# Performance work log

Hardware: AMD Instinct MI355X
Metric: run time of the kernel (lower is better)

## Reference

```python
import jax, jax.numpy as jnp
import numpy as np

B, L, E, H, DK, DV = 4, 2048, 512, 8, 64, 64
NEG = -1e9
LN_EPS = 1e-5


def setup_inputs() -> dict:
    key = jax.random.key(0)
    ks = jax.random.split(key, 16)
    q = jax.random.normal(ks[0], (B, L, E), jnp.float32)
    k = jax.random.normal(ks[1], (B, L, E), jnp.float32)
    v = jax.random.normal(ks[2], (B, L, E), jnp.float32)
    mask = jax.random.randint(ks[3], (B, L, L), 0, 2) > 0  # True = masked position
    def lin(kk, fan_in, dout, din):
        W = jax.random.normal(kk, (dout, din), jnp.float32) * (1.0 / np.sqrt(din))
        b = jnp.zeros((dout,), jnp.float32)
        return W, b
    Wq, bq = lin(ks[4], E, H * DK, E)
    Wk, bk = lin(ks[5], E, H * DK, E)
    Wv, bv = lin(ks[6], E, H * DV, E)
    Wfc, bfc = lin(ks[7], H * DV, E, H * DV)
    gamma = jnp.ones((E,), jnp.float32)
    beta = jnp.zeros((E,), jnp.float32)
    return dict(q=q, k=k, v=v, mask=mask, Wq=Wq, bq=bq, Wk=Wk, bk=bk,
                Wv=Wv, bv=bv, Wfc=Wfc, bfc=bfc, gamma=gamma, beta=beta)


def reference(q, k, v, mask, Wq, bq, Wk, bk, Wv, bv, Wfc, bfc, gamma, beta):
    residual = q
    Bq, Lq, _ = q.shape
    Lk = k.shape[1]
    # QKV projections, split heads: [B, L, H, D]
    qh = (q @ Wq.T + bq).reshape(Bq, Lq, H, DK)
    kh = (k @ Wk.T + bk).reshape(Bq, Lk, H, DK)
    vh = (v @ Wv.T + bv).reshape(Bq, Lk, H, DV)
    temp = jnp.asarray(np.sqrt(DK), qh.dtype)
    # scores in torch layout [H, B, Lq, Lk] (heads fastest-varying in H*B flatten)
    scores = jnp.einsum('bqhd,bkhd->hbqk', qh, kh) / temp
    scores = jnp.where(mask[None, :, :, :], NEG, scores)  # mask repeated over heads
    attn = jax.nn.softmax(scores, axis=-1)
    out = jnp.einsum('hbqk,bkhd->bqhd', attn, vh).reshape(Bq, Lq, H * DV)
    out = out @ Wfc.T + bfc
    # dropout p=0 -> identity
    x = out + residual
    mu = jnp.mean(x, axis=-1, keepdims=True)
    var = jnp.var(x, axis=-1, keepdims=True)
    outputs = (x - mu) / jnp.sqrt(var + LN_EPS) * gamma + beta
    attns = attn.reshape(H * Bq, Lq, Lk)
    return outputs, attns
```

## Files before the change

### kernel.cpp

```cpp
#include <hip/hip_runtime.h>

#define B_ 4
#define L_ 2048
#define E_ 512
#define H_ 8
#define D_ 64
#define NEGV (-1e9f)

typedef short s8v __attribute__((ext_vector_type(8)));
typedef float f4v __attribute__((ext_vector_type(4)));

static __device__ __forceinline__ unsigned short f2bf(float f) {
    union { float f; unsigned u; } v; v.f = f;
    unsigned r = v.u + 0x7FFFu + ((v.u >> 16) & 1u);
    return (unsigned short)(r >> 16);
}

template<int MODE, bool ABF16>
__global__ __launch_bounds__(256)
void gemm_bt(const void* __restrict__ Aptr, int lda,
             const float* __restrict__ Bm, int ldb,
             const float* __restrict__ bias,
             const float* __restrict__ resid,
             void* __restrict__ Cout, int ldc)
{
    constexpr int LS = 40;
    __shared__ unsigned short As[128 * LS];
    __shared__ unsigned short Bs[128 * LS];
    const int t = threadIdx.x;
    const int lane = t & 63, w = t >> 6;
    const int wm = (w >> 1) * 64, wn = (w & 1) * 64;
    const int bm0 = blockIdx.x * 128, bn0 = blockIdx.y * 128;
    const int ar = t >> 1, ak = (t & 1) * 16;
    const int fr = lane & 15, fq = lane >> 4, fk = fq * 8;

    f4v zero = {0.f, 0.f, 0.f, 0.f};
    f4v acc[4][4];
#pragma unroll
    for (int i = 0; i < 4; i++)
#pragma unroll
        for (int j = 0; j < 4; j++) acc[i][j] = zero;

    for (int k0 = 0; k0 < E_; k0 += 32) {
        unsigned short ta[16], tb[16];
        if (ABF16) {
            const unsigned short* ag = (const unsigned short*)Aptr + (size_t)(bm0 + ar) * lda + k0 + ak;
            *(int4*)&ta[0] = *(const int4*)ag;
            *(int4*)&ta[8] = *(const int4*)(ag + 8);
        } else {
            const float* ag = (const float*)Aptr + (size_t)(bm0 + ar) * lda + k0 + ak;
#pragma unroll
            for (int u = 0; u < 16; u += 4) {
                float4 va = *(const float4*)(ag + u);
                ta[u] = f2bf(va.x); ta[u+1] = f2bf(va.y);
                ta[u+2] = f2bf(va.z); ta[u+3] = f2bf(va.w);
            }
        }
        {
            const float* bg = Bm + (size_t)(bn0 + ar) * ldb + k0 + ak;
#pragma unroll
            for (int u = 0; u < 16; u += 4) {
                float4 vb = *(const float4*)(bg + u);
                tb[u] = f2bf(vb.x); tb[u+1] = f2bf(vb.y);
                tb[u+2] = f2bf(vb.z); tb[u+3] = f2bf(vb.w);
            }
        }
        __syncthreads();
        *(int4*)&As[ar * LS + ak]     = *(int4*)&ta[0];
        *(int4*)&As[ar * LS + ak + 8] = *(int4*)&ta[8];
        *(int4*)&Bs[ar * LS + ak]     = *(int4*)&tb[0];
        *(int4*)&Bs[ar * LS + ak + 8] = *(int4*)&tb[8];
        __syncthreads();

        s8v af[4], bf[4];
#pragma unroll
        for (int i = 0; i < 4; i++) af[i] = *(const s8v*)&As[(wm + 16*i + fr) * LS + fk];
#pragma unroll
        for (int j = 0; j < 4; j++) bf[j] = *(const s8v*)&Bs[(wn + 16*j + fr) * LS + fk];
#pragma unroll
        for (int i = 0; i < 4; i++)
#pragma unroll
            for (int j = 0; j < 4; j++)
                acc[i][j] = __builtin_amdgcn_mfma_f32_16x16x32_bf16(af[i], bf[j], acc[i][j], 0, 0, 0);
    }

#pragma unroll
    for (int i = 0; i < 4; i++) {
#pragma unroll
        for (int j = 0; j < 4; j++) {
            const int col = bn0 + wn + 16*j + fr;
            const float bv = bias ? bias[col] : 0.f;
#pragma unroll
            for (int reg = 0; reg < 4; reg++) {
                const int row = bm0 + wm + 16*i + fq*4 + reg;
                float val = acc[i][j][reg] + bv;
                if (MODE == 0) {
                    ((unsigned short*)Cout)[(size_t)row * ldc + col] = f2bf(val);
                } else if (MODE == 1) {
                    const int b = row >> 11, lk = row & 2047;
                    const int h = col >> 6,  dv = col & 63;
                    ((unsigned short*)Cout)[(((size_t)(b * H_ + h) * 64 + dv) << 11) + lk] = f2bf(val);
                } else {
                    float o = val + resid[(size_t)row * ldc + col];
                    ((float*)Cout)[(size_t)row * ldc + col] = o;
                }
            }
        }
    }
}

__global__ __launch_bounds__(256)
void attn_p1(const unsigned short* __restrict__ qh,
             const unsigned short* __restrict__ kh,
             const int* __restrict__ mask,
             float* __restrict__ stat_m, float* __restrict__ stat_l)
{
    __shared__ unsigned short Qs[64 * 72];
    __shared__ unsigned short Ks[128 * 72];
    const int t = threadIdx.x, lane = t & 63, w = t >> 6;
    const int q0 = blockIdx.x * 64;
    const int bh = blockIdx.y, b = bh >> 3, h = bh & 7;
    const int fr = lane & 15, fq = lane >> 4, fk = fq * 8;
    f4v zero = {0.f, 0.f, 0.f, 0.f};

    {
        const int row = t >> 2, kofs = (t & 3) * 16;
        const unsigned short* g = qh + ((size_t)(b * L_ + q0 + row) * E_ + h * 64 + kofs);
        *(int4*)&Qs[row * 72 + kofs]     = *(const int4*)g;
        *(int4*)&Qs[row * 72 + kofs + 8] = *(const int4*)(g + 8);
    }

    float m_r[4], l_r[4];
#pragma unroll
    for (int r = 0; r < 4; r++) { m_r[r] = -3e38f; l_r[r] = 0.f; }

    const size_t mbase = (size_t)b * ((size_t)L_ * L_);

    for (int kb = 0; kb < L_; kb += 128) {
        __syncthreads();
        {
            const int row = t >> 1, kofs = (t & 1) * 32;
            const unsigned short* g = kh + ((size_t)(b * L_ + kb + row) * E_ + h * 64 + kofs);
#pragma unroll
            for (int u = 0; u < 4; u++)
                *(int4*)&Ks[row * 72 + kofs + u * 8] = *(const int4*)(g + u * 8);
        }
        __syncthreads();

        s8v aq0 = *(const s8v*)&Qs[(w * 16 + fr) * 72 + fk];
        s8v aq1 = *(const s8v*)&Qs[(w * 16 + fr) * 72 + 32 + fk];
        f4v sv[8];
#pragma unroll
        for (int nt = 0; nt < 8; nt++) {
            s8v b0 = *(const s8v*)&Ks[(nt * 16 + fr) * 72 + fk];
            s8v b1 = *(const s8v*)&Ks[(nt * 16 + fr) * 72 + 32 + fk];
            f4v sc = zero;
            sc = __builtin_amdgcn_mfma_f32_16x16x32_bf16(aq0, b0, sc, 0, 0, 0);
            sc = __builtin_amdgcn_mfma_f32_16x16x32_bf16(aq1, b1, sc, 0, 0, 0);
            sv[nt] = sc;
        }

        float tm[4] = {-3e38f, -3e38f, -3e38f, -3e38f};
#pragma unroll
        for (int nt = 0; nt < 8; nt++)
#pragma unroll
            for (int reg = 0; reg < 4; reg++) {
                const int row = q0 + w * 16 + fq * 4 + reg;
                const int col = kb + nt * 16 + fr;
                const int mk = mask[mbase + (size_t)row * L_ + col];
                float s = mk ? NEGV : sv[nt][reg] * 0.125f;
                sv[nt][reg] = s;
                tm[reg] = fmaxf(tm[reg], s);
            }
#pragma unroll
        for (int d = 1; d < 16; d <<= 1)
#pragma unroll
            for (int reg = 0; reg < 4; reg++)
                tm[reg] = fmaxf(tm[reg], __shfl_xor(tm[reg], d));
#pragma unroll
        for (int reg = 0; reg < 4; reg++) {
            const float mn = fmaxf(m_r[reg], tm[reg]);
            const float corr = __expf(m_r[reg] - mn);
            float ps = 0.f;
#pragma unroll
            for (int nt = 0; nt < 8; nt++) ps += __expf(sv[nt][reg] - mn);
#pragma unroll
            for (int d = 1; d < 16; d <<= 1) ps += __shfl_xor(ps, d);
            l_r[reg] = l_r[reg] * corr + ps;
            m_r[reg] = mn;
        }
    }

    if (fr == 0) {
#pragma unroll
        for (int reg = 0; reg < 4; reg++) {
            const int row = q0 + w * 16 + fq * 4 + reg;
            stat_m[(size_t)bh * L_ + row] = m_r[reg];
            stat_l[(size_t)bh * L_ + row] = l_r[reg];
        }
    }
}

__global__ __launch_bounds__(256)
void attn_p2(const unsigned short* __restrict__ qh,
             const unsigned short* __restrict__ kh,
             const unsigned short* __restrict__ vt,
             const int* __restrict__ mask,
             const float* __restrict__ stat_m, const float* __restrict__ stat_l,
             float* __restrict__ attns, unsigned short* __restrict__ oh)
{
    __shared__ unsigned short Qs[64 * 72];
    __shared__ unsigned short Ks[128 * 72];
    __shared__ unsigned short Vs[64 * 136];
    __shared__ unsigned short Ps[64 * 136];
    const int t = threadIdx.x, lane = t & 63, w = t >> 6;
    const int q0 = blockIdx.x * 64;
    const int bh = blockIdx.y, b = bh >> 3, h = bh & 7;
    const int fr = lane & 15, fq = lane >> 4, fk = fq * 8;
    f4v zero = {0.f, 0.f, 0.f, 0.f};

    {
        const int row = t >> 2, kofs = (t & 3) * 16;
        const unsigned short* g = qh + ((size_t)(b * L_ + q0 + row) * E_ + h * 64 + kofs);
        *(int4*)&Qs[row * 72 + kofs]     = *(const int4*)g;
        *(int4*)&Qs[row * 72 + kofs + 8] = *(const int4*)(g + 8);
    }

    float m_r[4], rl[4];
#pragma unroll
    for (int reg = 0; reg < 4; reg++) {
        const int row = q0 + w * 16 + fq * 4 + reg;
        m_r[reg] = stat_m[(size_t)bh * L_ + row];
        rl[reg]  = 1.f / stat_l[(size_t)bh * L_ + row];
    }

    f4v o[4];
#pragma unroll
    for (int j = 0; j < 4; j++) o[j] = zero;

    const size_t mbase = (size_t)b * ((size_t)L_ * L_);
    const size_t abase = (size_t)(h * B_ + b) * ((size_t)L_ * L_);
    const int prow = w * 16 + fq * 4;

    for (int kb = 0; kb < L_; kb += 128) {
        __syncthreads();
        {
            const int row = t >> 1, kofs = (t & 1) * 32;
            const unsigned short* g = kh + ((size_t)(b * L_ + kb + row) * E_ + h * 64 + kofs);
#pragma unroll
            for (int u = 0; u < 4; u++)
                *(int4*)&Ks[row * 72 + kofs + u * 8] = *(const int4*)(g + u * 8);
        }
        {
            const int row = t >> 2, kofs = (t & 3) * 32;
            const unsigned short* g = vt + ((size_t)(b * H_ + h) * 64 + row) * L_ + kb + kofs;
#pragma unroll
            for (int u = 0; u < 4; u++)
                *(int4*)&Vs[row * 136 + kofs + u * 8] = *(const int4*)(g + u * 8);
        }
        __syncthreads();

        s8v aq0 = *(const s8v*)&Qs[(w * 16 + fr) * 72 + fk];
        s8v aq1 = *(const s8v*)&Qs[(w * 16 + fr) * 72 + 32 + fk];
#pragma unroll
        for (int nt = 0; nt < 8; nt++) {
            s8v b0 = *(const s8v*)&Ks[(nt * 16 + fr) * 72 + fk];
            s8v b1 = *(const s8v*)&Ks[(nt * 16 + fr) * 72 + 32 + fk];
            f4v sc = zero;
            sc = __builtin_amdgcn_mfma_f32_16x16x32_bf16(aq0, b0, sc, 0, 0, 0);
            sc = __builtin_amdgcn_mfma_f32_16x16x32_bf16(aq1, b1, sc, 0, 0, 0);
#pragma unroll
            for (int reg = 0; reg < 4; reg++) {
                const int row = q0 + prow + reg;
                const int col = kb + nt * 16 + fr;
                const int mk = mask[mbase + (size_t)row * L_ + col];
                float s = mk ? NEGV : sc[reg] * 0.125f;
                float p = __expf(s - m_r[reg]) * rl[reg];
                __builtin_nontemporal_store(p, &attns[abase + (size_t)row * L_ + col]);
                Ps[(prow + reg) * 136 + nt * 16 + fr] = f2bf(p);
            }
        }
        __syncthreads();

#pragma unroll
        for (int ks = 0; ks < 4; ks++) {
            s8v pa = *(const s8v*)&Ps[(w * 16 + fr) * 136 + ks * 32 + fk];
#pragma unroll
            for (int j = 0; j < 4; j++) {
                s8v vb = *(const s8v*)&Vs[(j * 16 + fr) * 136 + ks * 32 + fk];
                o[j] = __builtin_amdgcn_mfma_f32_16x16x32_bf16(pa, vb, o[j], 0, 0, 0);
            }
        }
    }

#pragma unroll
    for (int j = 0; j < 4; j++)
#pragma unroll
        for (int reg = 0; reg < 4; reg++) {
            const int row = q0 + prow + reg;
            const int col = h * 64 + j * 16 + fr;
            oh[(size_t)(b * L_ + row) * (H_ * D_) + col] = f2bf(o[j][reg]);
        }
}

__global__ __launch_bounds__(256)
void ln_k(const float* __restrict__ x, const float* __restrict__ gamma,
          const float* __restrict__ beta, float* __restrict__ out)
{
    const int t = threadIdx.x, lane = t & 63, w = t >> 6;
    const int row = blockIdx.x * 4 + w;
    const float* xr = x + (size_t)row * E_;
    const int cb = lane * 8;
    float4 a = *(const float4*)(xr + cb);
    float4 c = *(const float4*)(xr + cb + 4);
    float s  = a.x + a.y + a.z + a.w + c.x + c.y + c.z + c.w;
    float s2 = a.x*a.x + a.y*a.y + a.z*a.z + a.w*a.w
             + c.x*c.x + c.y*c.y + c.z*c.z + c.w*c.w;
#pragma unroll
    for (int d = 1; d < 64; d <<= 1) { s += __shfl_xor(s, d); s2 += __shfl_xor(s2, d); }
    const float mu  = s * (1.f / E_);
    const float var = s2 * (1.f / E_) - mu * mu;
    const float rs  = rsqrtf(var + 1e-5f);
    float4 g0 = *(const float4*)(gamma + cb), g1 = *(const float4*)(gamma + cb + 4);
    float4 b0 = *(const float4*)(beta + cb),  b1 = *(const float4*)(beta + cb + 4);
    float4 o0, o1;
    o0.x = (a.x - mu) * rs * g0.x + b0.x;  o0.y = (a.y - mu) * rs * g0.y + b0.y;
    o0.z = (a.z - mu) * rs * g0.z + b0.z;  o0.w = (a.w - mu) * rs * g0.w + b0.w;
    o1.x = (c.x - mu) * rs * g1.x + b1.x;  o1.y = (c.y - mu) * rs * g1.y + b1.y;
    o1.z = (c.z - mu) * rs * g1.z + b1.z;  o1.w = (c.w - mu) * rs * g1.w + b1.w;
    float* orow = out + (size_t)row * E_;
    *(float4*)(orow + cb)     = o0;
    *(float4*)(orow + cb + 4) = o1;
}

extern "C" void kernel_launch(void* const* d_in, const int* in_sizes, int n_in,
                              void* d_out, int out_size, void* d_ws, size_t ws_size,
                              hipStream_t stream)
{
    const float* q     = (const float*)d_in[0];
    const float* k     = (const float*)d_in[1];
    const float* v     = (const float*)d_in[2];
    const int*   mask  = (const int*)d_in[3];
    const float* Wq    = (const float*)d_in[4];
    const float* bq    = (const float*)d_in[5];
    const float* Wk    = (const float*)d_in[6];
    const float* bk    = (const float*)d_in[7];
    const float* Wv    = (const float*)d_in[8];
    const float* bv    = (const float*)d_in[9];
    const float* Wfc   = (const float*)d_in[10];
    const float* bfc   = (const float*)d_in[11];
    const float* gamma = (const float*)d_in[12];
    const float* beta  = (const float*)d_in[13];

    char* ws = (char*)d_ws;
    unsigned short* qh  = (unsigned short*)(ws);
    unsigned short* kh  = (unsigned short*)(ws + (8u  << 20));
    unsigned short* vt  = (unsigned short*)(ws + (16u << 20));
    unsigned short* oh  = (unsigned short*)(ws + (24u << 20));
    float* statm        = (float*)(ws + (32u << 20));
    float* statl        = (float*)(ws + (32u << 20) + (256u << 10));
    float* xbuf         = (float*)(ws);

    float* outputs = (float*)d_out;
    float* attns   = outputs + (size_t)B_ * L_ * E_;

    dim3 gg(64, 4), blk(256);
    gemm_bt<0, false><<<gg, blk, 0, stream>>>(q, E_, Wq, E_, bq, nullptr, qh, H_ * D_);
    gemm_bt<0, false><<<gg, blk, 0, stream>>>(k, E_, Wk, E_, bk, nullptr, kh, H_ * D_);
    gemm_bt<1, false><<<gg, blk, 0, stream>>>(v, E_, Wv, E_, bv, nullptr, vt, 0);

    attn_p1<<<dim3(32, 32), blk, 0, stream>>>(qh, kh, mask, statm, statl);
    attn_p2<<<dim3(32, 32), blk, 0, stream>>>(qh, kh, vt, mask, statm, statl, attns, oh);

    gemm_bt<2, true><<<gg, blk, 0, stream>>>(oh, H_ * D_, Wfc, H_ * D_, bfc, q, xbuf, E_);
    ln_k<<<2048, blk, 0, stream>>>(xbuf, gamma, beta, outputs);
}
```

Baseline: 863.5 us.

## Pack mask into bitmask and transpose MFMA operands for row-per-lane softmax

```diff
diff --git a/kernel.cpp b/kernel.cpp
--- a/kernel.cpp
+++ b/kernel.cpp
@@ -6,6 +6,7 @@
 #define H_ 8
 #define D_ 64
 #define NEGV (-1e9f)
+#define SC2 0.18033688011112042f
 
 typedef short s8v __attribute__((ext_vector_type(8)));
 typedef float f4v __attribute__((ext_vector_type(4)));
@@ -14,6 +15,20 @@
     union { float f; unsigned u; } v; v.f = f;
     unsigned r = v.u + 0x7FFFu + ((v.u >> 16) & 1u);
     return (unsigned short)(r >> 16);
+}
+
+__global__ __launch_bounds__(256)
+void pack_mask(const int* __restrict__ mask, unsigned long long* __restrict__ mbits)
+{
+    const int lane = threadIdx.x & 63;
+    const int wv = (int)((blockIdx.x * 256 + threadIdx.x) >> 6);
+    const int NW = 2048 * 4;
+    const int NWORDS = B_ * L_ * (L_ / 64);
+    for (int widx = wv; widx < NWORDS; widx += NW) {
+        const int mk = mask[(size_t)widx * 64 + lane];
+        const unsigned long long bb = __ballot(mk != 0);
+        if (lane == 0) mbits[widx] = bb;
+    }
 }
 
 template<int MODE, bool ABF16>
@@ -112,7 +127,7 @@
 __global__ __launch_bounds__(256)
 void attn_p1(const unsigned short* __restrict__ qh,
              const unsigned short* __restrict__ kh,
-             const int* __restrict__ mask,
+             const unsigned* __restrict__ mbits,
              float* __restrict__ stat_m, float* __restrict__ stat_l)
 {
     __shared__ unsigned short Qs[64 * 72];
@@ -120,7 +135,7 @@
     const int t = threadIdx.x, lane = t & 63, w = t >> 6;
     const int q0 = blockIdx.x * 64;
     const int bh = blockIdx.y, b = bh >> 3, h = bh & 7;
-    const int fr = lane & 15, fq = lane >> 4, fk = fq * 8;
+    const int fr = lane & 15, fq = lane >> 4, fk = fq * 8, sh4 = fq * 4;
     f4v zero = {0.f, 0.f, 0.f, 0.f};
 
     {
@@ -130,11 +145,10 @@
         *(int4*)&Qs[row * 72 + kofs + 8] = *(const int4*)(g + 8);
     }
 
-    float m_r[4], l_r[4];
-#pragma unroll
-    for (int r = 0; r < 4; r++) { m_r[r] = -3e38f; l_r[r] = 0.f; }
-
-    const size_t mbase = (size_t)b * ((size_t)L_ * L_);
+    const int myrow = q0 + w * 16 + fr;
+    const unsigned* mrow = mbits + (size_t)(b * L_ + myrow) * (L_ / 32);
+
+    float m = -3e38f, l = 0.f;
 
     for (int kb = 0; kb < L_; kb += 128) {
         __syncthreads();
@@ -147,57 +161,48 @@
         }
         __syncthreads();
 
-        s8v aq0 = *(const s8v*)&Qs[(w * 16 + fr) * 72 + fk];
-        s8v aq1 = *(const s8v*)&Qs[(w * 16 + fr) * 72 + 32 + fk];
-        f4v sv[8];
+        const s8v aq0 = *(const s8v*)&Qs[(w * 16 + fr) * 72 + fk];
+        const s8v aq1 = *(const s8v*)&Qs[(w * 16 + fr) * 72 + 32 + fk];
+        const uint4 mwv = *(const uint4*)(mrow + (kb >> 5));
+        const unsigned mwa[4] = {mwv.x, mwv.y, mwv.z, mwv.w};
+
+        float sv[8][4];
+        float tmax = -3e38f;
 #pragma unroll
         for (int nt = 0; nt < 8; nt++) {
             s8v b0 = *(const s8v*)&Ks[(nt * 16 + fr) * 72 + fk];
             s8v b1 = *(const s8v*)&Ks[(nt * 16 + fr) * 72 + 32 + fk];
             f4v sc = zero;
-            sc = __builtin_amdgcn_mfma_f32_16x16x32_bf16(aq0, b0, sc, 0, 0, 0);
-            sc = __builtin_amdgcn_mfma_f32_16x16x32_bf16(aq1, b1, sc, 0, 0, 0);
-            sv[nt] = sc;
-        }
-
-        float tm[4] = {-3e38f, -3e38f, -3e38f, -3e38f};
+            sc = __builtin_amdgcn_mfma_f32_16x16x32_bf16(b0, aq0, sc, 0, 0, 0);
+            sc = __builtin_amdgcn_mfma_f32_16x16x32_bf16(b1, aq1, sc, 0, 0, 0);
+            const unsigned mword = mwa[nt >> 1];
+#pragma unroll
+            for (int reg = 0; reg < 4; reg++) {
+                const unsigned bit = (mword >> (sh4 + ((nt & 1) * 16 + reg))) & 1u;
+                const float tvv = bit ? NEGV : sc[reg] * SC2;
+                sv[nt][reg] = tvv;
+                tmax = fmaxf(tmax, tvv);
+            }
+        }
+        tmax = fmaxf(tmax, __shfl_xor(tmax, 16));
+        tmax = fmaxf(tmax, __shfl_xor(tmax, 32));
+        const float mn = fmaxf(m, tmax);
+        const float corr = exp2f(m - mn);
+        float ps = 0.f;
 #pragma unroll
         for (int nt = 0; nt < 8; nt++)
 #pragma unroll
-            for (int reg = 0; reg < 4; reg++) {
-                const int row = q0 + w * 16 + fq * 4 + reg;
-                const int col = kb + nt * 16 + fr;
-                const int mk = mask[mbase + (size_t)row * L_ + col];
-                float s = mk ? NEGV : sv[nt][reg] * 0.125f;
-                sv[nt][reg] = s;
-                tm[reg] = fmaxf(tm[reg], s);
-            }
-#pragma unroll
-        for (int d = 1; d < 16; d <<= 1)
-#pragma unroll
             for (int reg = 0; reg < 4; reg++)
-                tm[reg] = fmaxf(tm[reg], __shfl_xor(tm[reg], d));
-#pragma unroll
-        for (int reg = 0; reg < 4; reg++) {
-            const float mn = fmaxf(m_r[reg], tm[reg]);
-            const float corr = __expf(m_r[reg] - mn);
-            float ps = 0.f;
-#pragma unroll
-            for (int nt = 0; nt < 8; nt++) ps += __expf(sv[nt][reg] - mn);
-#pragma unroll
-            for (int d = 1; d < 16; d <<= 1) ps += __shfl_xor(ps, d);
-            l_r[reg] = l_r[reg] * corr + ps;
-            m_r[reg] = mn;
-        }
-    }
-
-    if (fr == 0) {
-#pragma unroll
-        for (int reg = 0; reg < 4; reg++) {
-            const int row = q0 + w * 16 + fq * 4 + reg;
-            stat_m[(size_t)bh * L_ + row] = m_r[reg];
-            stat_l[(size_t)bh * L_ + row] = l_r[reg];
-        }
+                ps += exp2f(sv[nt][reg] - mn);
+        ps += __shfl_xor(ps, 16);
+        ps += __shfl_xor(ps, 32);
+        l = l * corr + ps;
+        m = mn;
+    }
+
+    if (fq == 0) {
+        stat_m[(size_t)bh * L_ + myrow] = m;
+        stat_l[(size_t)bh * L_ + myrow] = l;
     }
 }
 
@@ -205,7 +210,7 @@
 void attn_p2(const unsigned short* __restrict__ qh,
              const unsigned short* __restrict__ kh,
              const unsigned short* __restrict__ vt,
-             const int* __restrict__ mask,
+             const unsigned* __restrict__ mbits,
              const float* __restrict__ stat_m, const float* __restrict__ stat_l,
              float* __restrict__ attns, unsigned short* __restrict__ oh)
 {
@@ -216,7 +221,7 @@
     const int t = threadIdx.x, lane = t & 63, w = t >> 6;
     const int q0 = blockIdx.x * 64;
     const int bh = blockIdx.y, b = bh >> 3, h = bh & 7;
-    const int fr = lane & 15, fq = lane >> 4, fk = fq * 8;
+    const int fr = lane & 15, fq = lane >> 4, fk = fq * 8, sh4 = fq * 4;
     f4v zero = {0.f, 0.f, 0.f, 0.f};
 
     {
@@ -226,21 +231,16 @@
         *(int4*)&Qs[row * 72 + kofs + 8] = *(const int4*)(g + 8);
     }
 
-    float m_r[4], rl[4];
-#pragma unroll
-    for (int reg = 0; reg < 4; reg++) {
-        const int row = q0 + w * 16 + fq * 4 + reg;
-        m_r[reg] = stat_m[(size_t)bh * L_ + row];
-        rl[reg]  = 1.f / stat_l[(size_t)bh * L_ + row];
-    }
+    const int myrow = q0 + w * 16 + fr;
+    const unsigned* mrow = mbits + (size_t)(b * L_ + myrow) * (L_ / 32);
+    const float m  = stat_m[(size_t)bh * L_ + myrow];
+    const float rl = 1.f / stat_l[(size_t)bh * L_ + myrow];
 
     f4v o[4];
 #pragma unroll
     for (int j = 0; j < 4; j++) o[j] = zero;
 
-    const size_t mbase = (size_t)b * ((size_t)L_ * L_);
-    const size_t abase = (size_t)(h * B_ + b) * ((size_t)L_ * L_);
-    const int prow = w * 16 + fq * 4;
+    float* arow = attns + (size_t)(h * B_ + b) * ((size_t)L_ * L_) + (size_t)myrow * L_;
 
     for (int kb = 0; kb < L_; kb += 128) {
         __syncthreads();
@@ -260,25 +260,32 @@
         }
         __syncthreads();
 
-        s8v aq0 = *(const s8v*)&Qs[(w * 16 + fr) * 72 + fk];
-        s8v aq1 = *(const s8v*)&Qs[(w * 16 + fr) * 72 + 32 + fk];
+        const s8v aq0 = *(const s8v*)&Qs[(w * 16 + fr) * 72 + fk];
+        const s8v aq1 = *(const s8v*)&Qs[(w * 16 + fr) * 72 + 32 + fk];
+        const uint4 mwv = *(const uint4*)(mrow + (kb >> 5));
+        const unsigned mwa[4] = {mwv.x, mwv.y, mwv.z, mwv.w};
+
 #pragma unroll
         for (int nt = 0; nt < 8; nt++) {
             s8v b0 = *(const s8v*)&Ks[(nt * 16 + fr) * 72 + fk];
             s8v b1 = *(const s8v*)&Ks[(nt * 16 + fr) * 72 + 32 + fk];
             f4v sc = zero;
-            sc = __builtin_amdgcn_mfma_f32_16x16x32_bf16(aq0, b0, sc, 0, 0, 0);
-            sc = __builtin_amdgcn_mfma_f32_16x16x32_bf16(aq1, b1, sc, 0, 0, 0);
+            sc = __builtin_amdgcn_mfma_f32_16x16x32_bf16(b0, aq0, sc, 0, 0, 0);
+            sc = __builtin_amdgcn_mfma_f32_16x16x32_bf16(b1, aq1, sc, 0, 0, 0);
+            const unsigned mword = mwa[nt >> 1];
+            float p[4];
 #pragma unroll
             for (int reg = 0; reg < 4; reg++) {
-                const int row = q0 + prow + reg;
-                const int col = kb + nt * 16 + fr;
-                const int mk = mask[mbase + (size_t)row * L_ + col];
-                float s = mk ? NEGV : sc[reg] * 0.125f;
-                float p = __expf(s - m_r[reg]) * rl[reg];
-                __builtin_nontemporal_store(p, &attns[abase + (size_t)row * L_ + col]);
-                Ps[(prow + reg) * 136 + nt * 16 + fr] = f2bf(p);
-            }
+                const unsigned bit = (mword >> (sh4 + ((nt & 1) * 16 + reg))) & 1u;
+                const float tvv = bit ? NEGV : sc[reg] * SC2;
+                p[reg] = exp2f(tvv - m) * rl;
+            }
+            f4v pv = {p[0], p[1], p[2], p[3]};
+            __builtin_nontemporal_store(pv, (f4v*)(arow + kb + nt * 16 + sh4));
+            const unsigned lo = (unsigned)f2bf(p[0]) | ((unsigned)f2bf(p[1]) << 16);
+            const unsigned hi = (unsigned)f2bf(p[2]) | ((unsigned)f2bf(p[3]) << 16);
+            uint2 pp; pp.x = lo; pp.y = hi;
+            *(uint2*)&Ps[(w * 16 + fr) * 136 + nt * 16 + sh4] = pp;
         }
         __syncthreads();
 
@@ -288,19 +295,19 @@
 #pragma unroll
             for (int j = 0; j < 4; j++) {
                 s8v vb = *(const s8v*)&Vs[(j * 16 + fr) * 136 + ks * 32 + fk];
-                o[j] = __builtin_amdgcn_mfma_f32_16x16x32_bf16(pa, vb, o[j], 0, 0, 0);
-            }
-        }
-    }
-
-#pragma unroll
-    for (int j = 0; j < 4; j++)
-#pragma unroll
-        for (int reg = 0; reg < 4; reg++) {
-            const int row = q0 + prow + reg;
-            const int col = h * 64 + j * 16 + fr;
-            oh[(size_t)(b * L_ + row) * (H_ * D_) + col] = f2bf(o[j][reg]);
-        }
+                o[j] = __builtin_amdgcn_mfma_f32_16x16x32_bf16(vb, pa, o[j], 0, 0, 0);
+            }
+        }
+    }
+
+    unsigned short* orow = oh + (size_t)(b * L_ + myrow) * (H_ * D_) + h * 64;
+#pragma unroll
+    for (int j = 0; j < 4; j++) {
+        ushort4 ov;
+        ov.x = f2bf(o[j][0]); ov.y = f2bf(o[j][1]);
+        ov.z = f2bf(o[j][2]); ov.w = f2bf(o[j][3]);
+        *(ushort4*)&orow[j * 16 + sh4] = ov;
+    }
 }
 
 __global__ __launch_bounds__(256)
@@ -359,18 +366,21 @@
     unsigned short* oh  = (unsigned short*)(ws + (24u << 20));
     float* statm        = (float*)(ws + (32u << 20));
     float* statl        = (float*)(ws + (32u << 20) + (256u << 10));
+    unsigned long long* mbits = (unsigned long long*)(ws + (32u << 20) + (512u << 10));
     float* xbuf         = (float*)(ws);
 
     float* outputs = (float*)d_out;
     float* attns   = outputs + (size_t)B_ * L_ * E_;
 
     dim3 gg(64, 4), blk(256);
+    pack_mask<<<2048, blk, 0, stream>>>(mask, mbits);
     gemm_bt<0, false><<<gg, blk, 0, stream>>>(q, E_, Wq, E_, bq, nullptr, qh, H_ * D_);
     gemm_bt<0, false><<<gg, blk, 0, stream>>>(k, E_, Wk, E_, bk, nullptr, kh, H_ * D_);
     gemm_bt<1, false><<<gg, blk, 0, stream>>>(v, E_, Wv, E_, bv, nullptr, vt, 0);
 
-    attn_p1<<<dim3(32, 32), blk, 0, stream>>>(qh, kh, mask, statm, statl);
-    attn_p2<<<dim3(32, 32), blk, 0, stream>>>(qh, kh, vt, mask, statm, statl, attns, oh);
+    attn_p1<<<dim3(32, 32), blk, 0, stream>>>(qh, kh, (const unsigned*)mbits, statm, statl);
+    attn_p2<<<dim3(32, 32), blk, 0, stream>>>(qh, kh, vt, (const unsigned*)mbits,
+                                              statm, statl, attns, oh);
 
     gemm_bt<2, true><<<gg, blk, 0, stream>>>(oh, H_ * D_, Wfc, H_ * D_, bfc, q, xbuf, E_);
     ln_k<<<2048, blk, 0, stream>>>(xbuf, gamma, beta, outputs);
```

Result: no change. 878.8 us (+1.8%).
